# Kernel optimization log

Measured on AMD Instinct MI355X. Metric: run time of the kernel, lower is better.

## Reference

```python
import jax, jax.numpy as jnp
import numpy as np

B, L, D, H = 2, 2048, 1024, 16
P = D // H  # head dim = 64


def setup_inputs() -> dict:
    key = jax.random.key(0)
    ks = jax.random.split(key, 9)
    s = 1.0 / np.sqrt(D)
    x = jax.random.normal(ks[0], (B, L, D), dtype=jnp.float32)
    Wq = jax.random.normal(ks[1], (D, D), dtype=jnp.float32) * s
    bq = jax.random.normal(ks[2], (D,), dtype=jnp.float32) * 0.02
    Wk = jax.random.normal(ks[3], (D, D), dtype=jnp.float32) * s
    bk = jax.random.normal(ks[4], (D,), dtype=jnp.float32) * 0.02
    Wv = jax.random.normal(ks[5], (D, D), dtype=jnp.float32) * s
    bv = jax.random.normal(ks[6], (D,), dtype=jnp.float32) * 0.02
    Wo = jax.random.normal(ks[7], (D, D), dtype=jnp.float32) * s
    bo = jax.random.normal(ks[8], (D,), dtype=jnp.float32) * 0.02
    return {"token_activations": x, "Wq": Wq, "bq": bq, "Wk": Wk, "bk": bk,
            "Wv": Wv, "bv": bv, "Wo": Wo, "bo": bo}


def _split_heads(t):
    # 'b l (h p) -> b h l p'
    b, l, d = t.shape
    return t.reshape(b, l, H, P).transpose(0, 2, 1, 3)


def reference(token_activations, Wq, bq, Wk, bk, Wv, bv, Wo, bo):
    x = token_activations
    q = _split_heads(x @ Wq.T + bq)  # [B,H,L,P]
    k = _split_heads(x @ Wk.T + bk)
    v = _split_heads(x @ Wv.T + bv)
    # pattern[b,h,l,m] = K_l . Q_m / sqrt(P)
    scores = jnp.einsum('bhlp,bhmp->bhlm', k, q) / jnp.sqrt(jnp.float32(P))
    attn = jax.nn.softmax(scores, axis=-2)  # softmax over key axis l
    # out at query position m: sum_l attn[l,m] * V_l
    o = jnp.einsum('bhlm,bhlp->bhmp', attn, v)  # [B,H,L,P] (m indexed)
    o = o.transpose(0, 2, 1, 3).reshape(x.shape[0], x.shape[1], D)  # 'b h m p -> b m (h p)'
    return o @ Wo.T + bo
```

## Files before the change

### kernel.cpp

```cpp
#include <hip/hip_runtime.h>

typedef unsigned short u16;
typedef float f32x4 __attribute__((ext_vector_type(4)));
typedef __bf16 bf16x8 __attribute__((ext_vector_type(8)));
typedef __bf16 bf16x4 __attribute__((ext_vector_type(4)));

#define DEV static __device__ __forceinline__

constexpr int kB = 2;
constexpr int kL = 2048;
constexpr int kD = 1024;
constexpr int kH = 16;
constexpr int kP = 64;
constexpr int kM = kB * kL;
constexpr float kQScale = 0.125f * 1.44269504088896f;

DEV u16 f2bf(float x) {
  union { float f; unsigned u; } v;
  v.f = x;
  unsigned r = v.u + 0x7fffu + ((v.u >> 16) & 1u);
  return (u16)(r >> 16);
}

DEV void gload16(const void* g, void* l) {
  __builtin_amdgcn_global_load_lds(
      (const __attribute__((address_space(1))) unsigned int*)g,
      (__attribute__((address_space(3))) unsigned int*)l, 16, 0, 0);
}

__global__ void cvt_kernel(const float* __restrict__ src, u16* __restrict__ dst, int n4) {
  int i = blockIdx.x * blockDim.x + threadIdx.x;
  if (i >= n4) return;
  float4 v = reinterpret_cast<const float4*>(src)[i];
  uint2 o;
  o.x = (unsigned)f2bf(v.x) | ((unsigned)f2bf(v.y) << 16);
  o.y = (unsigned)f2bf(v.z) | ((unsigned)f2bf(v.w) << 16);
  reinterpret_cast<uint2*>(dst)[i] = o;
}

__global__ void cvtw_kernel(const float* __restrict__ w0, const float* __restrict__ w1,
                            const float* __restrict__ w2, const float* __restrict__ w3,
                            u16* __restrict__ o0, u16* __restrict__ o1,
                            u16* __restrict__ o2, u16* __restrict__ o3) {
  int sel = blockIdx.x >> 10;
  int i = (blockIdx.x & 1023) * 256 + threadIdx.x;
  const float* src = sel == 0 ? w0 : (sel == 1 ? w1 : (sel == 2 ? w2 : w3));
  u16* dst = sel == 0 ? o0 : (sel == 1 ? o1 : (sel == 2 ? o2 : o3));
  float4 v = reinterpret_cast<const float4*>(src)[i];
  uint2 o;
  o.x = (unsigned)f2bf(v.x) | ((unsigned)f2bf(v.y) << 16);
  o.y = (unsigned)f2bf(v.z) | ((unsigned)f2bf(v.w) << 16);
  reinterpret_cast<uint2*>(dst)[i] = o;
}

template <bool SWAP>
DEV void gemm_tile(const u16* __restrict__ A, const u16* __restrict__ W,
                   int m0, int n0, u16* As, u16* Bs, f32x4 acc[4][4]) {
  const int tid = threadIdx.x;
  const int w = tid >> 6, lane = tid & 63;
  const int wr = w >> 1, wc = w & 1;
  const int g = lane >> 4, c = lane & 15;
  const int srow = lane >> 2;
  const int skoff = ((lane & 3) ^ (srow & 3)) * 8;
  const int rsl0 = (g ^ (c & 3)) * 8;

  for (int k0 = 0; k0 < kD; k0 += 32) {
    __syncthreads();
#pragma unroll
    for (int j = 0; j < 2; ++j) {
      const u16* ga = A + (size_t)(m0 + w * 32 + j * 16 + srow) * kD + k0 + skoff;
      gload16(ga, As + (w * 32 + j * 16) * 32);
      const u16* gb = W + (size_t)(n0 + w * 32 + j * 16 + srow) * kD + k0 + skoff;
      gload16(gb, Bs + (w * 32 + j * 16) * 32);
    }
    __syncthreads();

    bf16x8 af[4], bfr[4];
#pragma unroll
    for (int f = 0; f < 4; ++f) {
      af[f]  = *reinterpret_cast<const bf16x8*>(As + (wr * 64 + f * 16 + c) * 32 + rsl0);
      bfr[f] = *reinterpret_cast<const bf16x8*>(Bs + (wc * 64 + f * 16 + c) * 32 + rsl0);
    }
#pragma unroll
    for (int fi = 0; fi < 4; ++fi)
#pragma unroll
      for (int fj = 0; fj < 4; ++fj) {
        if constexpr (SWAP)
          acc[fj][fi] = __builtin_amdgcn_mfma_f32_16x16x32_bf16(bfr[fj], af[fi], acc[fj][fi], 0, 0, 0);
        else
          acc[fi][fj] = __builtin_amdgcn_mfma_f32_16x16x32_bf16(af[fi], bfr[fj], acc[fi][fj], 0, 0, 0);
      }
  }
}

__global__ __launch_bounds__(256) void qkv_kernel(
    const u16* __restrict__ xb,
    const u16* __restrict__ wq, const u16* __restrict__ wk, const u16* __restrict__ wv,
    const float* __restrict__ bq, const float* __restrict__ bk, const float* __restrict__ bv,
    u16* __restrict__ qb, u16* __restrict__ kb, u16* __restrict__ vtb) {
  __shared__ u16 As[128 * 32], Bs[128 * 32];
  const int mb = blockIdx.x, nb = blockIdx.y;
  const int sel = nb >> 3;
  const int m0 = mb * 128, n0 = (nb & 7) * 128;
  const u16* W = sel == 0 ? wq : (sel == 1 ? wk : wv);
  const float* bias = sel == 0 ? bq : (sel == 1 ? bk : bv);

  const int lane = threadIdx.x & 63, w = threadIdx.x >> 6;
  const int wr = w >> 1, wc = w & 1, g = lane >> 4, c = lane & 15;
  const int bb = m0 >> 11;
  const int lbase = (m0 & 2047) + wr * 64;

  f32x4 acc[4][4];
#pragma unroll
  for (int i = 0; i < 4; ++i)
#pragma unroll
    for (int j = 0; j < 4; ++j) acc[i][j] = f32x4{0.f, 0.f, 0.f, 0.f};

  if (sel < 2) {
    gemm_tile<true>(xb, W, m0, n0, As, Bs, acc);
    u16* dst = sel == 0 ? qb : kb;
    const float scale = (sel == 0) ? kQScale : 1.0f;
#pragma unroll
    for (int fj = 0; fj < 4; ++fj) {
      const int n4 = n0 + wc * 64 + fj * 16 + g * 4;
      const float4 b4 = *reinterpret_cast<const float4*>(&bias[n4]);
      const int hh = n4 >> 6, p0 = n4 & 63;
      u16* base = dst + ((size_t)(bb * kH + hh)) * kL * kP + p0;
#pragma unroll
      for (int fi = 0; fi < 4; ++fi) {
        const int l = lbase + fi * 16 + c;
        bf16x4 o;
        o[0] = (__bf16)((acc[fj][fi][0] + b4.x) * scale);
        o[1] = (__bf16)((acc[fj][fi][1] + b4.y) * scale);
        o[2] = (__bf16)((acc[fj][fi][2] + b4.z) * scale);
        o[3] = (__bf16)((acc[fj][fi][3] + b4.w) * scale);
        *reinterpret_cast<bf16x4*>(base + (size_t)l * kP) = o;
      }
    }
  } else {
    gemm_tile<false>(xb, W, m0, n0, As, Bs, acc);
#pragma unroll
    for (int fj = 0; fj < 4; ++fj) {
      const int n = n0 + wc * 64 + fj * 16 + c;
      const float bv_ = bias[n];
      const int hh = n >> 6, p = n & 63;
      u16* base = vtb + (((size_t)(bb * kH + hh)) * kP + p) * kL;
#pragma unroll
      for (int fi = 0; fi < 4; ++fi) {
        const int l4 = lbase + fi * 16 + g * 4;
        bf16x4 o;
#pragma unroll
        for (int r = 0; r < 4; ++r) o[r] = (__bf16)(acc[fi][fj][r] + bv_);
        *reinterpret_cast<bf16x4*>(base + l4) = o;
      }
    }
  }
}

__global__ __launch_bounds__(256) void out_kernel(
    const u16* __restrict__ ob, const u16* __restrict__ wo,
    const float* __restrict__ bo, float* __restrict__ out) {
  __shared__ u16 As[128 * 32], Bs[128 * 32];
  const int m0 = blockIdx.x * 128, n0 = blockIdx.y * 128;
  f32x4 acc[4][4];
#pragma unroll
  for (int i = 0; i < 4; ++i)
#pragma unroll
    for (int j = 0; j < 4; ++j) acc[i][j] = f32x4{0.f, 0.f, 0.f, 0.f};

  gemm_tile<true>(ob, wo, m0, n0, As, Bs, acc);

  const int lane = threadIdx.x & 63, w = threadIdx.x >> 6;
  const int wr = w >> 1, wc = w & 1, g = lane >> 4, c = lane & 15;
#pragma unroll
  for (int fj = 0; fj < 4; ++fj) {
    const int n4 = n0 + wc * 64 + fj * 16 + g * 4;
    const float4 b4 = *reinterpret_cast<const float4*>(&bo[n4]);
#pragma unroll
    for (int fi = 0; fi < 4; ++fi) {
      const int m = m0 + wr * 64 + fi * 16 + c;
      float4 o;
      o.x = acc[fj][fi][0] + b4.x;
      o.y = acc[fj][fi][1] + b4.y;
      o.z = acc[fj][fi][2] + b4.z;
      o.w = acc[fj][fi][3] + b4.w;
      *reinterpret_cast<float4*>(&out[(size_t)m * kD + n4]) = o;
    }
  }
}

__global__ __launch_bounds__(512, 2) void attn_kernel(
    const u16* __restrict__ qb, const u16* __restrict__ kb,
    const u16* __restrict__ vtb, u16* __restrict__ ob) {
  __shared__ __align__(16) char kvs[2][2][8192];
  __shared__ __align__(16) char pts[8][2048];
  const int tid = threadIdx.x, w = tid >> 6, lane = tid & 63;
  const int g = lane >> 4, c = lane & 15;
  const int h = blockIdx.y, b = blockIdx.z;
  const size_t hoff = ((size_t)(b * kH + h)) * kL * kP;
  const char* Qg = (const char*)(qb + hoff);
  const char* Kg = (const char*)(kb + hoff);
  const char* Vg = (const char*)(vtb + hoff);
  const int q0 = blockIdx.x * 128 + w * 16;

  const int lrow = lane >> 3;
  const int spb = ((lane & 7) ^ lrow) << 4;
  const char* kp = Kg + (size_t)(w * 8 + lrow) * 128 + spb;
  const char* vp = Vg + (size_t)(w * 8 + lrow) * (kL * 2) + spb;

  auto stage = [&](int buf) {
    gload16(kp, &kvs[buf][0][w * 1024]);
    gload16(vp, &kvs[buf][1][w * 1024]);
    kp += 64 * 128;
    vp += 128;
  };

  const int csw = (c & 7) << 4;
  const int kvb0 = c * 128 + ((g * 16) ^ csw);
  const int kvb1 = c * 128 + ((64 + g * 16) ^ csw);
  char* myPt = &pts[w][0];

  bf16x8 qf[2];
#pragma unroll
  for (int kc = 0; kc < 2; ++kc)
    qf[kc] = *reinterpret_cast<const bf16x8*>(Qg + (size_t)(q0 + c) * 128 + kc * 64 + g * 16);

  f32x4 oacc[4];
#pragma unroll
  for (int pt = 0; pt < 4; ++pt) oacc[pt] = f32x4{0.f, 0.f, 0.f, 0.f};
  float Srun = 0.f;

  stage(0);
  __syncthreads();

  constexpr int NT = kL / 64;
  auto body = [&](int cur, int t) {
    if (t + 1 < NT) stage(cur ^ 1);
    const char* Ks = &kvs[cur][0][0];
    const char* Vs = &kvs[cur][1][0];

    f32x4 s[4];
    __builtin_amdgcn_s_setprio(1);
#pragma unroll
    for (int lt = 0; lt < 4; ++lt) {
      bf16x8 k0 = *reinterpret_cast<const bf16x8*>(Ks + lt * 2048 + kvb0);
      bf16x8 k1 = *reinterpret_cast<const bf16x8*>(Ks + lt * 2048 + kvb1);
      f32x4 z = f32x4{0.f, 0.f, 0.f, 0.f};
      z = __builtin_amdgcn_mfma_f32_16x16x32_bf16(k0, qf[0], z, 0, 0, 0);
      z = __builtin_amdgcn_mfma_f32_16x16x32_bf16(k1, qf[1], z, 0, 0, 0);
      s[lt] = z;
    }
    __builtin_amdgcn_s_setprio(0);

    float tsum = 0.f;
#pragma unroll
    for (int lt = 0; lt < 4; ++lt) {
      bf16x4 pv;
#pragma unroll
      for (int r = 0; r < 4; ++r) {
        float p = __builtin_amdgcn_exp2f(s[lt][r]);
        tsum += p;
        pv[r] = (__bf16)p;
      }
      *reinterpret_cast<bf16x4*>(myPt + c * 128 + ((lt * 32 + g * 8) ^ csw)) = pv;
    }
    Srun += tsum;

    bf16x8 pf0 = *reinterpret_cast<const bf16x8*>(myPt + kvb0);
    bf16x8 pf1 = *reinterpret_cast<const bf16x8*>(myPt + kvb1);
    __builtin_amdgcn_s_setprio(1);
#pragma unroll
    for (int pt = 0; pt < 4; ++pt) {
      bf16x8 v0 = *reinterpret_cast<const bf16x8*>(Vs + pt * 2048 + kvb0);
      bf16x8 v1 = *reinterpret_cast<const bf16x8*>(Vs + pt * 2048 + kvb1);
      oacc[pt] = __builtin_amdgcn_mfma_f32_16x16x32_bf16(pf0, v0, oacc[pt], 0, 0, 0);
      oacc[pt] = __builtin_amdgcn_mfma_f32_16x16x32_bf16(pf1, v1, oacc[pt], 0, 0, 0);
    }
    __builtin_amdgcn_s_setprio(0);
    __syncthreads();
  };

  for (int t = 0; t < NT; t += 2) {
    body(0, t);
    body(1, t + 1);
  }

  Srun += __shfl_xor(Srun, 16, 64);
  Srun += __shfl_xor(Srun, 32, 64);

  float rs = 1.f / Srun;
  float fr[4];
#pragma unroll
  for (int r = 0; r < 4; ++r) fr[r] = __shfl(rs, g * 4 + r, 64);
#pragma unroll
  for (int pt = 0; pt < 4; ++pt)
#pragma unroll
    for (int r = 0; r < 4; ++r) {
      int q = q0 + g * 4 + r;
      ob[((size_t)(b * kL + q)) * kD + h * kP + pt * 16 + c] = f2bf(oacc[pt][r] * fr[r]);
    }
}

extern "C" void kernel_launch(void* const* d_in, const int* in_sizes, int n_in,
                              void* d_out, int out_size, void* d_ws, size_t ws_size,
                              hipStream_t stream) {
  (void)in_sizes; (void)n_in; (void)out_size; (void)ws_size;
  const float* x  = (const float*)d_in[0];
  const float* Wq = (const float*)d_in[1];
  const float* bq = (const float*)d_in[2];
  const float* Wk = (const float*)d_in[3];
  const float* bk = (const float*)d_in[4];
  const float* Wv = (const float*)d_in[5];
  const float* bv = (const float*)d_in[6];
  const float* Wo = (const float*)d_in[7];
  const float* bo = (const float*)d_in[8];
  float* out = (float*)d_out;

  char* ws = (char*)d_ws;
  u16* xb  = (u16*)(ws);
  u16* wqb = (u16*)(ws + (8u << 20));
  u16* wkb = (u16*)(ws + (10u << 20));
  u16* wvb = (u16*)(ws + (12u << 20));
  u16* wob = (u16*)(ws + (14u << 20));
  u16* qb  = (u16*)(ws + (16u << 20));
  u16* kb  = (u16*)(ws + (24u << 20));
  u16* vtb = (u16*)(ws + (32u << 20));

  cvt_kernel<<<kM * kD / 1024, 256, 0, stream>>>(x, xb, kM * kD / 4);
  cvtw_kernel<<<4096, 256, 0, stream>>>(Wq, Wk, Wv, Wo, wqb, wkb, wvb, wob);

  qkv_kernel<<<dim3(kM / 128, 24), 256, 0, stream>>>(
      xb, wqb, wkb, wvb, bq, bk, bv, qb, kb, vtb);

  attn_kernel<<<dim3(kL / 128, kH, kB), 512, 0, stream>>>(qb, kb, vtb, xb);

  out_kernel<<<dim3(kM / 128, kD / 128), 256, 0, stream>>>(xb, wob, bo, out);
}
```

Baseline: 117.6 us.

## Triple-buffer attention K/V loads and widen GEMM K-step to 64

The attention kernel moves from double to triple buffering of K/V tiles in shared memory. It uses explicit vmcnt waits plus raw barriers so the next tile's loads stay in flight while the current tile is computed, which removes a full __syncthreads per tile. Separately, the projection GEMM tile loads 64-wide K slices with an XOR swizzle over 8 chunks, halving the number of barrier pairs per GEMM. This costs more LDS per block (which may lower occupancy) and relies on correct hand-coded waitcnt counts and on the unrolled loop matching NT=32.

```diff
diff --git a/kernel.cpp b/kernel.cpp
--- a/kernel.cpp
+++ b/kernel.cpp
@@ -60,36 +60,41 @@
   const int w = tid >> 6, lane = tid & 63;
   const int wr = w >> 1, wc = w & 1;
   const int g = lane >> 4, c = lane & 15;
-  const int srow = lane >> 2;
-  const int skoff = ((lane & 3) ^ (srow & 3)) * 8;
-  const int rsl0 = (g ^ (c & 3)) * 8;
-
-  for (int k0 = 0; k0 < kD; k0 += 32) {
+  const int srow = lane >> 3;
+  const int sel0 = ((lane & 7) ^ srow) * 8;
+  const int csw = (c & 7) << 4;
+
+  for (int k0 = 0; k0 < kD; k0 += 64) {
     __syncthreads();
 #pragma unroll
-    for (int j = 0; j < 2; ++j) {
-      const u16* ga = A + (size_t)(m0 + w * 32 + j * 16 + srow) * kD + k0 + skoff;
-      gload16(ga, As + (w * 32 + j * 16) * 32);
-      const u16* gb = W + (size_t)(n0 + w * 32 + j * 16 + srow) * kD + k0 + skoff;
-      gload16(gb, Bs + (w * 32 + j * 16) * 32);
+    for (int j = 0; j < 4; ++j) {
+      const int row = w * 32 + j * 8;
+      const u16* ga = A + (size_t)(m0 + row + srow) * kD + k0 + sel0;
+      gload16(ga, As + row * 64);
+      const u16* gb = W + (size_t)(n0 + row + srow) * kD + k0 + sel0;
+      gload16(gb, Bs + row * 64);
     }
     __syncthreads();
 
-    bf16x8 af[4], bfr[4];
-#pragma unroll
-    for (int f = 0; f < 4; ++f) {
-      af[f]  = *reinterpret_cast<const bf16x8*>(As + (wr * 64 + f * 16 + c) * 32 + rsl0);
-      bfr[f] = *reinterpret_cast<const bf16x8*>(Bs + (wc * 64 + f * 16 + c) * 32 + rsl0);
-    }
-#pragma unroll
-    for (int fi = 0; fi < 4; ++fi)
-#pragma unroll
-      for (int fj = 0; fj < 4; ++fj) {
-        if constexpr (SWAP)
-          acc[fj][fi] = __builtin_amdgcn_mfma_f32_16x16x32_bf16(bfr[fj], af[fi], acc[fj][fi], 0, 0, 0);
-        else
-          acc[fi][fj] = __builtin_amdgcn_mfma_f32_16x16x32_bf16(af[fi], bfr[fj], acc[fi][fj], 0, 0, 0);
+#pragma unroll
+    for (int kc = 0; kc < 2; ++kc) {
+      const int rb = ((kc * 64 + g * 16) ^ csw) >> 1;
+      bf16x8 af[4], bfr[4];
+#pragma unroll
+      for (int f = 0; f < 4; ++f) {
+        af[f]  = *reinterpret_cast<const bf16x8*>(As + (wr * 64 + f * 16 + c) * 64 + rb);
+        bfr[f] = *reinterpret_cast<const bf16x8*>(Bs + (wc * 64 + f * 16 + c) * 64 + rb);
       }
+#pragma unroll
+      for (int fi = 0; fi < 4; ++fi)
+#pragma unroll
+        for (int fj = 0; fj < 4; ++fj) {
+          if constexpr (SWAP)
+            acc[fj][fi] = __builtin_amdgcn_mfma_f32_16x16x32_bf16(bfr[fj], af[fi], acc[fj][fi], 0, 0, 0);
+          else
+            acc[fi][fj] = __builtin_amdgcn_mfma_f32_16x16x32_bf16(af[fi], bfr[fj], acc[fi][fj], 0, 0, 0);
+        }
+    }
   }
 }
 
@@ -98,7 +103,7 @@
     const u16* __restrict__ wq, const u16* __restrict__ wk, const u16* __restrict__ wv,
     const float* __restrict__ bq, const float* __restrict__ bk, const float* __restrict__ bv,
     u16* __restrict__ qb, u16* __restrict__ kb, u16* __restrict__ vtb) {
-  __shared__ u16 As[128 * 32], Bs[128 * 32];
+  __shared__ u16 As[128 * 64], Bs[128 * 64];
   const int mb = blockIdx.x, nb = blockIdx.y;
   const int sel = nb >> 3;
   const int m0 = mb * 128, n0 = (nb & 7) * 128;
@@ -160,7 +165,7 @@
 __global__ __launch_bounds__(256) void out_kernel(
     const u16* __restrict__ ob, const u16* __restrict__ wo,
     const float* __restrict__ bo, float* __restrict__ out) {
-  __shared__ u16 As[128 * 32], Bs[128 * 32];
+  __shared__ u16 As[128 * 64], Bs[128 * 64];
   const int m0 = blockIdx.x * 128, n0 = blockIdx.y * 128;
   f32x4 acc[4][4];
 #pragma unroll
@@ -192,7 +197,7 @@
 __global__ __launch_bounds__(512, 2) void attn_kernel(
     const u16* __restrict__ qb, const u16* __restrict__ kb,
     const u16* __restrict__ vtb, u16* __restrict__ ob) {
-  __shared__ __align__(16) char kvs[2][2][8192];
+  __shared__ __align__(16) char kvs[3][2][8192];
   __shared__ __align__(16) char pts[8][2048];
   const int tid = threadIdx.x, w = tid >> 6, lane = tid & 63;
   const int g = lane >> 4, c = lane & 15;
@@ -230,12 +235,7 @@
   for (int pt = 0; pt < 4; ++pt) oacc[pt] = f32x4{0.f, 0.f, 0.f, 0.f};
   float Srun = 0.f;
 
-  stage(0);
-  __syncthreads();
-
-  constexpr int NT = kL / 64;
-  auto body = [&](int cur, int t) {
-    if (t + 1 < NT) stage(cur ^ 1);
+  auto compute = [&](int cur) {
     const char* Ks = &kvs[cur][0][0];
     const char* Vs = &kvs[cur][1][0];
 
@@ -277,13 +277,24 @@
       oacc[pt] = __builtin_amdgcn_mfma_f32_16x16x32_bf16(pf1, v1, oacc[pt], 0, 0, 0);
     }
     __builtin_amdgcn_s_setprio(0);
-    __syncthreads();
   };
 
-  for (int t = 0; t < NT; t += 2) {
-    body(0, t);
-    body(1, t + 1);
+#define WAITV2 asm volatile("s_waitcnt vmcnt(2)" ::: "memory")
+#define WAITV0 asm volatile("s_waitcnt vmcnt(0)" ::: "memory")
+
+  stage(0);
+  stage(1);
+
+  for (int t = 0; t < 30; t += 3) {
+    WAITV2; __builtin_amdgcn_s_barrier(); stage(2); compute(0);
+    WAITV2; __builtin_amdgcn_s_barrier(); stage(0); compute(1);
+    WAITV2; __builtin_amdgcn_s_barrier(); stage(1); compute(2);
   }
+  WAITV2; __builtin_amdgcn_s_barrier(); compute(0);
+  WAITV0; __builtin_amdgcn_s_barrier(); compute(1);
+
+#undef WAITV2
+#undef WAITV0
 
   Srun += __shfl_xor(Srun, 16, 64);
   Srun += __shfl_xor(Srun, 32, 64);
```

Result: slower. 134.1 us (+14.0%).

## Switch attention kernel to 32x32x16 MFMA with 4 waves of 32 queries each

Applied to the files above, without the earlier changes.

The attention kernel now uses 32x32x16 bf16 MFMA tiles instead of 16x16x32. Each of 4 waves handles 32 query rows rather than 8 waves handling 16, and the block size drops from 512 to 256 threads. Larger MFMA tiles reuse each LDS fragment across more work and cut LDS reads per flop, and fewer waves share each K/V stage. The cost is more accumulator registers per wave, a different P-tile layout in LDS, and reduced wave-level parallelism per block.

```diff
diff --git a/kernel.cpp b/kernel.cpp
--- a/kernel.cpp
+++ b/kernel.cpp
@@ -2,6 +2,7 @@
 
 typedef unsigned short u16;
 typedef float f32x4 __attribute__((ext_vector_type(4)));
+typedef float f32x16 __attribute__((ext_vector_type(16)));
 typedef __bf16 bf16x8 __attribute__((ext_vector_type(8)));
 typedef __bf16 bf16x4 __attribute__((ext_vector_type(4)));
 
@@ -189,46 +190,55 @@
   }
 }
 
-__global__ __launch_bounds__(512, 2) void attn_kernel(
+__global__ __launch_bounds__(256, 3) void attn_kernel(
     const u16* __restrict__ qb, const u16* __restrict__ kb,
     const u16* __restrict__ vtb, u16* __restrict__ ob) {
   __shared__ __align__(16) char kvs[2][2][8192];
-  __shared__ __align__(16) char pts[8][2048];
+  __shared__ __align__(16) char pts[4][4096];
   const int tid = threadIdx.x, w = tid >> 6, lane = tid & 63;
-  const int g = lane >> 4, c = lane & 15;
+  const int lq = lane & 31, hi = lane >> 5;
   const int h = blockIdx.y, b = blockIdx.z;
   const size_t hoff = ((size_t)(b * kH + h)) * kL * kP;
   const char* Qg = (const char*)(qb + hoff);
   const char* Kg = (const char*)(kb + hoff);
   const char* Vg = (const char*)(vtb + hoff);
-  const int q0 = blockIdx.x * 128 + w * 16;
+  const int q0 = blockIdx.x * 128 + w * 32;
 
   const int lrow = lane >> 3;
   const int spb = ((lane & 7) ^ lrow) << 4;
-  const char* kp = Kg + (size_t)(w * 8 + lrow) * 128 + spb;
-  const char* vp = Vg + (size_t)(w * 8 + lrow) * (kL * 2) + spb;
+  const char* kp0 = Kg + (size_t)(w * 16 + lrow) * 128 + spb;
+  const char* kp1 = Kg + (size_t)(w * 16 + 8 + lrow) * 128 + spb;
+  const char* vp0 = Vg + (size_t)(w * 16 + lrow) * (kL * 2) + spb;
+  const char* vp1 = Vg + (size_t)(w * 16 + 8 + lrow) * (kL * 2) + spb;
 
   auto stage = [&](int buf) {
-    gload16(kp, &kvs[buf][0][w * 1024]);
-    gload16(vp, &kvs[buf][1][w * 1024]);
-    kp += 64 * 128;
-    vp += 128;
+    gload16(kp0, &kvs[buf][0][w * 2048]);
+    gload16(kp1, &kvs[buf][0][w * 2048 + 1024]);
+    gload16(vp0, &kvs[buf][1][w * 2048]);
+    gload16(vp1, &kvs[buf][1][w * 2048 + 1024]);
+    kp0 += 64 * 128; kp1 += 64 * 128;
+    vp0 += 128;      vp1 += 128;
   };
 
-  const int csw = (c & 7) << 4;
-  const int kvb0 = c * 128 + ((g * 16) ^ csw);
-  const int kvb1 = c * 128 + ((64 + g * 16) ^ csw);
+  const int rsw = (lq & 7) << 4;
+  int kbase[4];
+#pragma unroll
+  for (int kk = 0; kk < 4; ++kk)
+    kbase[kk] = lq * 128 + ((kk * 32 + hi * 16) ^ rsw);
   char* myPt = &pts[w][0];
 
-  bf16x8 qf[2];
-#pragma unroll
-  for (int kc = 0; kc < 2; ++kc)
-    qf[kc] = *reinterpret_cast<const bf16x8*>(Qg + (size_t)(q0 + c) * 128 + kc * 64 + g * 16);
-
-  f32x4 oacc[4];
-#pragma unroll
-  for (int pt = 0; pt < 4; ++pt) oacc[pt] = f32x4{0.f, 0.f, 0.f, 0.f};
-  float Srun = 0.f;
+  bf16x8 qf[4];
+#pragma unroll
+  for (int kk = 0; kk < 4; ++kk)
+    qf[kk] = *reinterpret_cast<const bf16x8*>(
+        Qg + (size_t)(q0 + lq) * 128 + kk * 32 + hi * 16);
+
+  f32x16 oacc[2];
+#pragma unroll
+  for (int ot = 0; ot < 2; ++ot)
+#pragma unroll
+    for (int r = 0; r < 16; ++r) oacc[ot][r] = 0.f;
+  f32x4 srun4 = f32x4{0.f, 0.f, 0.f, 0.f};
 
   stage(0);
   __syncthreads();
@@ -239,42 +249,46 @@
     const char* Ks = &kvs[cur][0][0];
     const char* Vs = &kvs[cur][1][0];
 
-    f32x4 s[4];
+    f32x16 s[2];
     __builtin_amdgcn_s_setprio(1);
 #pragma unroll
-    for (int lt = 0; lt < 4; ++lt) {
-      bf16x8 k0 = *reinterpret_cast<const bf16x8*>(Ks + lt * 2048 + kvb0);
-      bf16x8 k1 = *reinterpret_cast<const bf16x8*>(Ks + lt * 2048 + kvb1);
-      f32x4 z = f32x4{0.f, 0.f, 0.f, 0.f};
-      z = __builtin_amdgcn_mfma_f32_16x16x32_bf16(k0, qf[0], z, 0, 0, 0);
-      z = __builtin_amdgcn_mfma_f32_16x16x32_bf16(k1, qf[1], z, 0, 0, 0);
-      s[lt] = z;
+    for (int ot = 0; ot < 2; ++ot) {
+      f32x16 z;
+#pragma unroll
+      for (int r = 0; r < 16; ++r) z[r] = 0.f;
+#pragma unroll
+      for (int kk = 0; kk < 4; ++kk) {
+        bf16x8 kf = *reinterpret_cast<const bf16x8*>(Ks + ot * 4096 + kbase[kk]);
+        z = __builtin_amdgcn_mfma_f32_32x32x16_bf16(kf, qf[kk], z, 0, 0, 0);
+      }
+      s[ot] = z;
     }
     __builtin_amdgcn_s_setprio(0);
 
-    float tsum = 0.f;
-#pragma unroll
-    for (int lt = 0; lt < 4; ++lt) {
-      bf16x4 pv;
-#pragma unroll
-      for (int r = 0; r < 4; ++r) {
-        float p = __builtin_amdgcn_exp2f(s[lt][r]);
-        tsum += p;
-        pv[r] = (__bf16)p;
-      }
-      *reinterpret_cast<bf16x4*>(myPt + c * 128 + ((lt * 32 + g * 8) ^ csw)) = pv;
-    }
-    Srun += tsum;
-
-    bf16x8 pf0 = *reinterpret_cast<const bf16x8*>(myPt + kvb0);
-    bf16x8 pf1 = *reinterpret_cast<const bf16x8*>(myPt + kvb1);
+#pragma unroll
+    for (int ot = 0; ot < 2; ++ot)
+#pragma unroll
+      for (int a = 0; a < 4; ++a) {
+        bf16x4 pv;
+#pragma unroll
+        for (int i = 0; i < 4; ++i) {
+          float p = __builtin_amdgcn_exp2f(s[ot][a * 4 + i]);
+          srun4[i] += p;
+          pv[i] = (__bf16)p;
+        }
+        *reinterpret_cast<bf16x4*>(
+            myPt + lq * 128 + ((ot * 64 + a * 16 + hi * 8) ^ rsw)) = pv;
+      }
+
     __builtin_amdgcn_s_setprio(1);
 #pragma unroll
-    for (int pt = 0; pt < 4; ++pt) {
-      bf16x8 v0 = *reinterpret_cast<const bf16x8*>(Vs + pt * 2048 + kvb0);
-      bf16x8 v1 = *reinterpret_cast<const bf16x8*>(Vs + pt * 2048 + kvb1);
-      oacc[pt] = __builtin_amdgcn_mfma_f32_16x16x32_bf16(pf0, v0, oacc[pt], 0, 0, 0);
-      oacc[pt] = __builtin_amdgcn_mfma_f32_16x16x32_bf16(pf1, v1, oacc[pt], 0, 0, 0);
+    for (int ot = 0; ot < 2; ++ot) {
+#pragma unroll
+      for (int kk = 0; kk < 4; ++kk) {
+        bf16x8 pf = *reinterpret_cast<const bf16x8*>(myPt + kbase[kk]);
+        bf16x8 vf = *reinterpret_cast<const bf16x8*>(Vs + ot * 4096 + kbase[kk]);
+        oacc[ot] = __builtin_amdgcn_mfma_f32_32x32x16_bf16(pf, vf, oacc[ot], 0, 0, 0);
+      }
     }
     __builtin_amdgcn_s_setprio(0);
     __syncthreads();
@@ -285,19 +299,18 @@
     body(1, t + 1);
   }
 
-  Srun += __shfl_xor(Srun, 16, 64);
+  float Srun = srun4[0] + srun4[1] + srun4[2] + srun4[3];
   Srun += __shfl_xor(Srun, 32, 64);
-
-  float rs = 1.f / Srun;
-  float fr[4];
-#pragma unroll
-  for (int r = 0; r < 4; ++r) fr[r] = __shfl(rs, g * 4 + r, 64);
-#pragma unroll
-  for (int pt = 0; pt < 4; ++pt)
-#pragma unroll
-    for (int r = 0; r < 4; ++r) {
-      int q = q0 + g * 4 + r;
-      ob[((size_t)(b * kL + q)) * kD + h * kP + pt * 16 + c] = f2bf(oacc[pt][r] * fr[r]);
+  float rsAll = 1.f / Srun;
+
+#pragma unroll
+  for (int ot = 0; ot < 2; ++ot)
+#pragma unroll
+    for (int r = 0; r < 16; ++r) {
+      const int q = (r & 3) + 8 * (r >> 2) + 4 * hi;
+      const float rs = __shfl(rsAll, q, 64);
+      ob[((size_t)(b * kL + q0 + q)) * kD + h * kP + ot * 32 + lq] =
+          f2bf(oacc[ot][r] * rs);
     }
 }
 
@@ -332,7 +345,7 @@
   qkv_kernel<<<dim3(kM / 128, 24), 256, 0, stream>>>(
       xb, wqb, wkb, wvb, bq, bk, bv, qb, kb, vtb);
 
-  attn_kernel<<<dim3(kL / 128, kH, kB), 512, 0, stream>>>(qb, kb, vtb, xb);
+  attn_kernel<<<dim3(kL / 128, kH, kB), 256, 0, stream>>>(qb, kb, vtb, xb);
 
   out_kernel<<<dim3(kM / 128, kD / 128), 256, 0, stream>>>(xb, wob, bo, out);
 }
```

Measured after the change: 120.6 us. 1.03x slower.
